# Performance work log

Hardware: AMD Instinct MI355X
Metric: run time of the kernel (lower is better)

Reference implementation:

```python
import jax, jax.numpy as jnp
import numpy as np

N, E, B = 10000, 160000, 256
IN, DESC = 57, 1217
# (in_dim, heads, out_per_head) for the 4 GATConv layers
CONV_DIMS = [(57, 5, 114), (570, 5, 171), (855, 5, 114), (570, 1, 570)]
FC_DIMS = [(1024 + DESC, 1024), (1024, 2048), (2048, 1024), (1024, 256), (256, 1)]


def setup_inputs() -> dict:
    key = jax.random.key(0)
    cnt = [0]
    def p(shape, scale=0.05):
        cnt[0] += 1
        return jax.random.normal(jax.random.fold_in(key, cnt[0]), shape, jnp.float32) * scale
    d = {}
    d["x"] = jax.random.normal(jax.random.fold_in(key, 100), (N, IN), jnp.float32)
    d["edge_index"] = jax.random.randint(jax.random.fold_in(key, 101), (2, E), 0, N)
    d["batch"] = jnp.sort(jax.random.randint(jax.random.fold_in(key, 102), (N,), 0, B))
    d["desc"] = jax.random.normal(jax.random.fold_in(key, 103), (B, DESC), jnp.float32)
    for i, (ci, H, C) in enumerate(CONV_DIMS, 1):
        d[f"W{i}"] = p((ci, H * C))
        d[f"as{i}"] = p((H, C))
        d[f"ad{i}"] = p((H, C))
        d[f"b{i}"] = jnp.zeros((H * C,), jnp.float32)
    d["Wg"] = p((570, 1024)); d["bg"] = jnp.zeros((1024,), jnp.float32)
    for i, (ci, co) in enumerate(FC_DIMS, 1):
        d[f"Wf{i}"] = p((ci, co))
        d[f"bf{i}"] = jnp.zeros((co,), jnp.float32)
    return d


def gat_conv(x, src, dst, W, a_src, a_dst, b):
    """PyG GATConv (eval mode: attention dropout off), self-loops already in src/dst."""
    n = x.shape[0]
    H, C = a_src.shape
    h = (x @ W).reshape(n, H, C)                      # [N,H,C]
    al_s = (h * a_src).sum(-1)                         # [N,H]
    al_d = (h * a_dst).sum(-1)                         # [N,H]
    e = jax.nn.leaky_relu(al_s[src] + al_d[dst], 0.2)  # [E,H]
    # segment softmax over destination node
    m = jax.ops.segment_max(e, dst, num_segments=n)
    e = jnp.exp(e - m[dst])
    s = jax.ops.segment_sum(e, dst, num_segments=n)
    alpha = e / (s[dst] + 1e-16)                       # [E,H]
    msg = h[src] * alpha[:, :, None]                   # [E,H,C]
    out = jax.ops.segment_sum(msg, dst, num_segments=n)
    return out.reshape(n, H * C) + b


def reference(x, edge_index, batch, desc,
              W1, as1, ad1, b1, W2, as2, ad2, b2,
              W3, as3, ad3, b3, W4, as4, ad4, b4,
              Wg, bg, Wf1, bf1, Wf2, bf2, Wf3, bf3, Wf4, bf4, Wf5, bf5):
    n = x.shape[0]
    loops = jnp.arange(n)
    src = jnp.concatenate([edge_index[0], loops])
    dst = jnp.concatenate([edge_index[1], loops])
    h = x
    for W, a_s, a_d, b in [(W1, as1, ad1, b1), (W2, as2, ad2, b2),
                           (W3, as3, ad3, b3), (W4, as4, ad4, b4)]:
        h = jax.nn.relu(gat_conv(h, src, dst, W, a_s, a_d, b))
    pooled = jax.ops.segment_sum(h, batch, num_segments=B)   # global_add_pool [B,570]
    g = pooled @ Wg + bg
    z = jnp.concatenate([g, desc], axis=1)                    # [B, 2241]
    z = jax.nn.relu(z @ Wf1 + bf1)
    z = jax.nn.relu(z @ Wf2 + bf2)
    z = jax.nn.relu(z @ Wf3 + bf3)
    z = jax.nn.relu(z @ Wf4 + bf4)
    return z @ Wf5 + bf5                                      # [B,1]
```

## Files before the change

### kernel.cpp

```cpp
#include <hip/hip_runtime.h>
#include <hip/hip_bf16.h>
#include <math.h>

#define NNODES 10000
#define NEDGES 160000
#define NB     256
#define ETOT   (NEDGES + NNODES)
#define INDIM  57
#define DESCD  1217

static inline size_t align256(size_t x) { return (x + 255) & ~size_t(255); }

typedef _Float16 half8_t __attribute__((ext_vector_type(8)));
typedef float f32x4 __attribute__((ext_vector_type(4)));

__device__ inline float wave_max(float v) {
#pragma unroll
  for (int o = 32; o > 0; o >>= 1) v = fmaxf(v, __shfl_xor(v, o));
  return v;
}
__device__ inline float wave_sum(float v) {
#pragma unroll
  for (int o = 32; o > 0; o >>= 1) v += __shfl_xor(v, o);
  return v;
}

__global__ void count_kernel(const int* __restrict__ ei, int* __restrict__ deg) {
  int e = blockIdx.x * blockDim.x + threadIdx.x;
  if (e < ETOT) {
    int dst = (e < NEDGES) ? ei[NEDGES + e] : (e - NEDGES);
    atomicAdd(&deg[dst], 1);
  }
}

__global__ __launch_bounds__(1024) void scan_kernel(const int* __restrict__ deg,
                                                    int* __restrict__ row_ptr,
                                                    int* __restrict__ cursor) {
  __shared__ int part[1024];
  const int CHUNK = (NNODES + 1023) / 1024;
  int t = threadIdx.x;
  int start = t * CHUNK;
  int sum = 0;
  for (int i = 0; i < CHUNK; ++i) {
    int idx = start + i;
    if (idx < NNODES) sum += deg[idx];
  }
  part[t] = sum;
  __syncthreads();
  for (int off = 1; off < 1024; off <<= 1) {
    int v = (t >= off) ? part[t - off] : 0;
    __syncthreads();
    part[t] += v;
    __syncthreads();
  }
  int run = (t > 0) ? part[t - 1] : 0;
  for (int i = 0; i < CHUNK; ++i) {
    int idx = start + i;
    if (idx < NNODES) {
      row_ptr[idx] = run;
      cursor[idx] = run;
      run += deg[idx];
    }
  }
  if (t == 1023) row_ptr[NNODES] = ETOT;
}

__global__ void scatter_kernel(const int* __restrict__ ei, int* __restrict__ cursor,
                               int* __restrict__ csr_src) {
  int e = blockIdx.x * blockDim.x + threadIdx.x;
  if (e < ETOT) {
    int src, dst;
    if (e < NEDGES) { src = ei[e]; dst = ei[NEDGES + e]; }
    else            { src = e - NEDGES; dst = src; }
    int idx = atomicAdd(&cursor[dst], 1);
    csr_src[idx] = src;
  }
}

__global__ void convert_x_kernel(const float* __restrict__ x, _Float16* __restrict__ x16) {
  int t = blockIdx.x * blockDim.x + threadIdx.x;
  if (t >= NNODES * 64) return;
  int n = t >> 6, k = t & 63;
  x16[t] = (_Float16)((k < INDIM) ? x[n * INDIM + k] : 0.f);
}

__global__ void convert_wt_kernel(const float* __restrict__ W, _Float16* __restrict__ Wt,
                                  int K, int N, int Kpad, int Npad) {
  int t = blockIdx.x * blockDim.x + threadIdx.x;
  if (t >= Npad * Kpad) return;
  int n = t / Kpad, k = t - n * Kpad;
  float v = (n < N && k < K) ? W[(size_t)k * N + n] : 0.f;
  Wt[t] = (_Float16)v;
}

__global__ void pooled16_kernel(const float* __restrict__ pooled, _Float16* __restrict__ p16) {
  int t = blockIdx.x * blockDim.x + threadIdx.x;
  if (t >= NB * 576) return;
  int b = t / 576, c = t - b * 576;
  p16[t] = (_Float16)((c < 570) ? pooled[b * 570 + c] : 0.f);
}

__global__ void desc_fill_kernel(const float* __restrict__ desc, _Float16* __restrict__ z16) {
  int t = blockIdx.x * blockDim.x + threadIdx.x;
  if (t >= NB * 1280) return;
  int b = t / 1280, i = t - b * 1280;
  z16[(size_t)b * 2304 + 1024 + i] = (_Float16)((i < DESCD) ? desc[b * DESCD + i] : 0.f);
}

__global__ __launch_bounds__(256) void mfma_gemm_kernel(
    const _Float16* __restrict__ A, const _Float16* __restrict__ Bt,
    _Float16* __restrict__ C, int M, int Kpad, int Nreal, int ldc) {
  __shared__ __align__(16) char smem[32768];
  char* AsB = smem;
  char* BsB = smem + 16384;
  int tid = threadIdx.x;
  int lane = tid & 63, wid = tid >> 6;
  int l15 = lane & 15, g = lane >> 4;
  int wr = wid >> 1, wc = wid & 1;
  int m0 = blockIdx.y * 128, n0 = blockIdx.x * 128;
  f32x4 acc[4][4];
#pragma unroll
  for (int i = 0; i < 4; ++i)
#pragma unroll
    for (int j = 0; j < 4; ++j) acc[i][j] = (f32x4){0.f, 0.f, 0.f, 0.f};

  int KT = Kpad >> 6;
  half8_t pa[4], pb[4];
#pragma unroll
  for (int i = 0; i < 4; ++i) {
    int r = i * 32 + (tid >> 3);
    int cs = (tid & 7) ^ (r & 7);
    int ga = min(m0 + r, M - 1);
    pa[i] = *(const half8_t*)(A + (size_t)ga * Kpad + cs * 8);
    pb[i] = *(const half8_t*)(Bt + (size_t)(n0 + r) * Kpad + cs * 8);
  }
  for (int kt = 0; kt < KT; ++kt) {
    __syncthreads();
#pragma unroll
    for (int i = 0; i < 4; ++i) {
      *(half8_t*)(AsB + i * 4096 + tid * 16) = pa[i];
      *(half8_t*)(BsB + i * 4096 + tid * 16) = pb[i];
    }
    __syncthreads();
    if (kt + 1 < KT) {
      int k0 = (kt + 1) << 6;
#pragma unroll
      for (int i = 0; i < 4; ++i) {
        int r = i * 32 + (tid >> 3);
        int cs = (tid & 7) ^ (r & 7);
        int ga = min(m0 + r, M - 1);
        pa[i] = *(const half8_t*)(A + (size_t)ga * Kpad + k0 + cs * 8);
        pb[i] = *(const half8_t*)(Bt + (size_t)(n0 + r) * Kpad + k0 + cs * 8);
      }
    }
#pragma unroll
    for (int kk = 0; kk < 2; ++kk) {
      half8_t af[4], bf[4];
#pragma unroll
      for (int f = 0; f < 4; ++f) {
        int ra = wr * 64 + f * 16 + l15;
        af[f] = *(const half8_t*)(AsB + ra * 128 + (((kk * 4 + g) ^ (ra & 7)) << 4));
        int cb = wc * 64 + f * 16 + l15;
        bf[f] = *(const half8_t*)(BsB + cb * 128 + (((kk * 4 + g) ^ (cb & 7)) << 4));
      }
#pragma unroll
      for (int fm = 0; fm < 4; ++fm)
#pragma unroll
        for (int fn = 0; fn < 4; ++fn)
          acc[fm][fn] = __builtin_amdgcn_mfma_f32_16x16x32_f16(af[fm], bf[fn], acc[fm][fn], 0, 0, 0);
    }
  }
#pragma unroll
  for (int fm = 0; fm < 4; ++fm) {
    int gmb = m0 + wr * 64 + fm * 16 + g * 4;
#pragma unroll
    for (int fn = 0; fn < 4; ++fn) {
      int gn = n0 + wc * 64 + fn * 16 + l15;
      if (gn >= Nreal) continue;
#pragma unroll
      for (int j = 0; j < 4; ++j) {
        int gm = gmb + j;
        if (gm < M) C[(size_t)gm * ldc + gn] = (_Float16)acc[fm][fn][j];
      }
    }
  }
}

__global__ __launch_bounds__(256) void mfma_splitk_kernel(
    const _Float16* __restrict__ A, const _Float16* __restrict__ Bt,
    float* __restrict__ P, int M, int Kpad, int N, int ktpc) {
  __shared__ __align__(16) char smem[32768];
  char* AsB = smem;
  char* BsB = smem + 16384;
  int tid = threadIdx.x;
  int lane = tid & 63, wid = tid >> 6;
  int l15 = lane & 15, g = lane >> 4;
  int wr = wid >> 1, wc = wid & 1;
  int m0 = blockIdx.y * 128, n0 = blockIdx.x * 128;
  int z = blockIdx.z;
  int KT = Kpad >> 6;
  int ktb = z * ktpc;
  int kte = min(KT, ktb + ktpc);
  f32x4 acc[4][4];
#pragma unroll
  for (int i = 0; i < 4; ++i)
#pragma unroll
    for (int j = 0; j < 4; ++j) acc[i][j] = (f32x4){0.f, 0.f, 0.f, 0.f};

  half8_t pa[4], pb[4];
  {
    int k0 = ktb << 6;
#pragma unroll
    for (int i = 0; i < 4; ++i) {
      int r = i * 32 + (tid >> 3);
      int cs = (tid & 7) ^ (r & 7);
      int ga = min(m0 + r, M - 1);
      pa[i] = *(const half8_t*)(A + (size_t)ga * Kpad + k0 + cs * 8);
      pb[i] = *(const half8_t*)(Bt + (size_t)(n0 + r) * Kpad + k0 + cs * 8);
    }
  }
  for (int kt = ktb; kt < kte; ++kt) {
    __syncthreads();
#pragma unroll
    for (int i = 0; i < 4; ++i) {
      *(half8_t*)(AsB + i * 4096 + tid * 16) = pa[i];
      *(half8_t*)(BsB + i * 4096 + tid * 16) = pb[i];
    }
    __syncthreads();
    if (kt + 1 < kte) {
      int k0 = (kt + 1) << 6;
#pragma unroll
      for (int i = 0; i < 4; ++i) {
        int r = i * 32 + (tid >> 3);
        int cs = (tid & 7) ^ (r & 7);
        int ga = min(m0 + r, M - 1);
        pa[i] = *(const half8_t*)(A + (size_t)ga * Kpad + k0 + cs * 8);
        pb[i] = *(const half8_t*)(Bt + (size_t)(n0 + r) * Kpad + k0 + cs * 8);
      }
    }
#pragma unroll
    for (int kk = 0; kk < 2; ++kk) {
      half8_t af[4], bf[4];
#pragma unroll
      for (int f = 0; f < 4; ++f) {
        int ra = wr * 64 + f * 16 + l15;
        af[f] = *(const half8_t*)(AsB + ra * 128 + (((kk * 4 + g) ^ (ra & 7)) << 4));
        int cb = wc * 64 + f * 16 + l15;
        bf[f] = *(const half8_t*)(BsB + cb * 128 + (((kk * 4 + g) ^ (cb & 7)) << 4));
      }
#pragma unroll
      for (int fm = 0; fm < 4; ++fm)
#pragma unroll
        for (int fn = 0; fn < 4; ++fn)
          acc[fm][fn] = __builtin_amdgcn_mfma_f32_16x16x32_f16(af[fm], bf[fn], acc[fm][fn], 0, 0, 0);
    }
  }
  size_t zb = (size_t)z * M;
#pragma unroll
  for (int fm = 0; fm < 4; ++fm) {
    int gmb = m0 + wr * 64 + fm * 16 + g * 4;
#pragma unroll
    for (int fn = 0; fn < 4; ++fn) {
      int gn = n0 + wc * 64 + fn * 16 + l15;
      if (gn >= N) continue;
#pragma unroll
      for (int j = 0; j < 4; ++j) {
        int gm = gmb + j;
        if (gm < M) P[(zb + gm) * N + gn] = acc[fm][fn][j];
      }
    }
  }
}

__global__ void reduce16_kernel(const float* __restrict__ P, const float* __restrict__ bias,
                                _Float16* __restrict__ O, int M, int N, int ldo,
                                int S, int relu) {
  int idx = blockIdx.x * blockDim.x + threadIdx.x;
  if (idx >= M * ldo) return;
  int row = idx / ldo, col = idx - row * ldo;
  if (col >= N) return;
  float s = bias[col];
  int MN = M * N;
  for (int z = 0; z < S; ++z) s += P[(size_t)z * MN + row * N + col];
  if (relu) s = fmaxf(s, 0.f);
  O[idx] = (_Float16)s;
}

__global__ __launch_bounds__(256) void fc5_kernel(const _Float16* __restrict__ A,
                                                  const float* __restrict__ w,
                                                  const float* __restrict__ b,
                                                  float* __restrict__ out) {
  int wid = threadIdx.x >> 6, lane = threadIdx.x & 63;
  int m = blockIdx.x * 4 + wid;
  if (m >= NB) return;
  float s = 0.f;
  for (int k = lane; k < 256; k += 64) s += (float)A[m * 256 + k] * w[k];
  s = wave_sum(s);
  if (lane == 0) out[m] = s + b[0];
}

__global__ __launch_bounds__(256) void al_kernel(const _Float16* __restrict__ hbuf,
                                                 const float* __restrict__ a_s,
                                                 const float* __restrict__ a_d,
                                                 float* __restrict__ als,
                                                 float* __restrict__ ald,
                                                 int H, int C, int ldh) {
  int wid = threadIdx.x >> 6, lane = threadIdx.x & 63;
  int g = blockIdx.x * 4 + wid;
  if (g >= NNODES * H) return;
  int n = g / H, h = g % H;
  const _Float16* hr = hbuf + (size_t)n * ldh + (size_t)h * C;
  float ss = 0.f, sd = 0.f;
  for (int c = lane; c < C; c += 64) {
    float v = (float)hr[c];
    ss += v * a_s[h * C + c];
    sd += v * a_d[h * C + c];
  }
  ss = wave_sum(ss);
  sd = wave_sum(sd);
  if (lane == 0) { als[g] = ss; ald[g] = sd; }
}

template <int H>
__global__ __launch_bounds__(256) void att_kernel_t(const float* __restrict__ als,
                                                    const float* __restrict__ ald,
                                                    const int* __restrict__ row_ptr,
                                                    const int* __restrict__ csr_src,
                                                    float* __restrict__ alpha) {
  int wid = threadIdx.x >> 6, lane = threadIdx.x & 63;
  int n = blockIdx.x * 4 + wid;
  if (n >= NNODES) return;
  int rp = row_ptr[n], deg = row_ptr[n + 1] - rp;
  float ad[H], m[H], e0[H], e1[H], ssum[H];
#pragma unroll
  for (int h = 0; h < H; ++h) { ad[h] = ald[n * H + h]; m[h] = -1e30f; ssum[h] = 0.f; }
  for (int j = lane, it = 0; j < deg; j += 64, ++it) {
    int s = csr_src[rp + j];
#pragma unroll
    for (int h = 0; h < H; ++h) {
      float e = als[s * H + h] + ad[h];
      e = (e >= 0.f) ? e : 0.2f * e;
      if (it == 0) e0[h] = e; else if (it == 1) e1[h] = e;
      m[h] = fmaxf(m[h], e);
    }
  }
#pragma unroll
  for (int h = 0; h < H; ++h) m[h] = wave_max(m[h]);
  for (int j = lane, it = 0; j < deg; j += 64, ++it) {
    int s = (it >= 2) ? csr_src[rp + j] : 0;
#pragma unroll
    for (int h = 0; h < H; ++h) {
      float e;
      if (it == 0) e = e0[h];
      else if (it == 1) e = e1[h];
      else { e = als[s * H + h] + ad[h]; e = (e >= 0.f) ? e : 0.2f * e; }
      ssum[h] += expf(e - m[h]);
    }
  }
#pragma unroll
  for (int h = 0; h < H; ++h) { ssum[h] = 1.f / (wave_sum(ssum[h]) + 1e-16f); }
  for (int j = lane, it = 0; j < deg; j += 64, ++it) {
    int s = (it >= 2) ? csr_src[rp + j] : 0;
#pragma unroll
    for (int h = 0; h < H; ++h) {
      float e;
      if (it == 0) e = e0[h];
      else if (it == 1) e = e1[h];
      else { e = als[s * H + h] + ad[h]; e = (e >= 0.f) ? e : 0.2f * e; }
      alpha[(size_t)(rp + j) * H + h] = expf(e - m[h]) * ssum[h];
    }
  }
}

__global__ __launch_bounds__(256) void agg_kernel(const _Float16* __restrict__ hbuf,
                                                  const float* __restrict__ alpha,
                                                  const int* __restrict__ row_ptr,
                                                  const int* __restrict__ csr_src,
                                                  const float* __restrict__ bias,
                                                  _Float16* __restrict__ h16o,
                                                  int H, int C, int ldh, int ldo,
                                                  int HC, int nchunks) {
  int wid = threadIdx.x >> 6, lane = threadIdx.x & 63;
  int gw = blockIdx.x * 4 + wid;
  int n = gw / nchunks, chunk = gw - n * nchunks;
  if (n >= NNODES) return;
  int k0 = chunk * 512 + lane * 8;
  if (k0 >= ldo) return;
  _Float16* op = h16o + (size_t)n * ldo + k0;
  if (k0 >= HC) { *(half8_t*)op = (half8_t){}; return; }
  int h0 = k0 / C;
  int h1 = min(k0 + 7, HC - 1) / C;
  int split = (h0 + 1) * C;
  int rp = row_ptr[n], deg = row_ptr[n + 1] - rp;
  float acc[8] = {};
#pragma unroll 2
  for (int j = 0; j < deg; ++j) {
    int e = rp + j;
    int s = csr_src[e];
    float a0 = alpha[(size_t)e * H + h0];
    float a1 = alpha[(size_t)e * H + h1];
    half8_t v = *(const half8_t*)(hbuf + (size_t)s * ldh + k0);
#pragma unroll
    for (int i = 0; i < 8; ++i)
      acc[i] += ((k0 + i < split) ? a0 : a1) * (float)v[i];
  }
  half8_t o;
#pragma unroll
  for (int i = 0; i < 8; ++i)
    o[i] = (_Float16)((k0 + i < HC) ? fmaxf(acc[i] + bias[k0 + i], 0.f) : 0.f);
  *(half8_t*)op = o;
}

__global__ __launch_bounds__(256) void pool_kernel(const _Float16* __restrict__ h4,
                                                   const int* __restrict__ batch,
                                                   float* __restrict__ pooled, int F, int ldh) {
  int wid = threadIdx.x >> 6, lane = threadIdx.x & 63;
  int n = blockIdx.x * 4 + wid;
  if (n >= NNODES) return;
  int b = batch[n];
  for (int k = lane; k < F; k += 64)
    atomicAdd(&pooled[(size_t)b * F + k], (float)h4[(size_t)n * ldh + k]);
}

extern "C" void kernel_launch(void* const* d_in, const int* in_sizes, int n_in,
                              void* d_out, int out_size, void* d_ws, size_t ws_size,
                              hipStream_t stream) {
  const float* x    = (const float*)d_in[0];
  const int*   ei   = (const int*)d_in[1];
  const int*   batch= (const int*)d_in[2];
  const float* desc = (const float*)d_in[3];
  const float* W1 = (const float*)d_in[4];  const float* as1 = (const float*)d_in[5];
  const float* ad1 = (const float*)d_in[6]; const float* b1 = (const float*)d_in[7];
  const float* W2 = (const float*)d_in[8];  const float* as2 = (const float*)d_in[9];
  const float* ad2 = (const float*)d_in[10];const float* b2 = (const float*)d_in[11];
  const float* W3 = (const float*)d_in[12]; const float* as3 = (const float*)d_in[13];
  const float* ad3 = (const float*)d_in[14];const float* b3 = (const float*)d_in[15];
  const float* W4 = (const float*)d_in[16]; const float* as4 = (const float*)d_in[17];
  const float* ad4 = (const float*)d_in[18];const float* b4 = (const float*)d_in[19];
  const float* Wg = (const float*)d_in[20]; const float* bg = (const float*)d_in[21];
  const float* Wf1 = (const float*)d_in[22];const float* bf1 = (const float*)d_in[23];
  const float* Wf2 = (const float*)d_in[24];const float* bf2 = (const float*)d_in[25];
  const float* Wf3 = (const float*)d_in[26];const float* bf3 = (const float*)d_in[27];
  const float* Wf4 = (const float*)d_in[28];const float* bf4 = (const float*)d_in[29];
  const float* Wf5 = (const float*)d_in[30];const float* bf5 = (const float*)d_in[31];
  float* out = (float*)d_out;

  char* p = (char*)d_ws;
  size_t off = 0;
  auto alloc = [&](size_t bytes) -> char* {
    char* r = p + off;
    off = align256(off + bytes);
    return r;
  };
  int*      deg     = (int*)alloc(sizeof(int) * NNODES);
  int*      row_ptr = (int*)alloc(sizeof(int) * (NNODES + 1));
  int*      cursor  = (int*)alloc(sizeof(int) * NNODES);
  int*      csr_src = (int*)alloc(sizeof(int) * ETOT);
  float*    als     = (float*)alloc(sizeof(float) * NNODES * 5);
  float*    ald     = (float*)alloc(sizeof(float) * NNODES * 5);
  float*    alpha   = (float*)alloc(sizeof(float) * (size_t)ETOT * 5);
  _Float16* x16     = (_Float16*)alloc(sizeof(_Float16) * (size_t)NNODES * 64);
  _Float16* hA16    = (_Float16*)alloc(sizeof(_Float16) * ((size_t)NNODES * 856 + 1024));
  _Float16* h16     = (_Float16*)alloc(sizeof(_Float16) * ((size_t)NNODES * 896 + 1024));
  _Float16* Wt      = (_Float16*)alloc(sizeof(_Float16) * 1024 * 2304);
  float*    pooled  = (float*)alloc(sizeof(float) * NB * 570);
  _Float16* p16     = (_Float16*)alloc(sizeof(_Float16) * NB * 576);
  _Float16* z16     = (_Float16*)alloc(sizeof(_Float16) * NB * 2304);
  _Float16* t16     = (_Float16*)alloc(sizeof(_Float16) * NB * 2048);
  _Float16* u16     = (_Float16*)alloc(sizeof(_Float16) * NB * 2048);
  _Float16* v16     = (_Float16*)alloc(sizeof(_Float16) * NB * 256);
  (void)ws_size;

  hipMemsetAsync(deg, 0, sizeof(int) * NNODES, stream);
  {
    dim3 g((ETOT + 255) / 256);
    count_kernel<<<g, 256, 0, stream>>>(ei, deg);
    scan_kernel<<<1, 1024, 0, stream>>>(deg, row_ptr, cursor);
    scatter_kernel<<<g, 256, 0, stream>>>(ei, cursor, csr_src);
  }
  convert_x_kernel<<<(NNODES * 64 + 255) / 256, 256, 0, stream>>>(x, x16);

  dim3 gnode((NNODES + 3) / 4);

  struct LayerDef { const float* W; const float* a_s; const float* a_d; const float* b;
                    int K; int H; int C; int Kpad; int Npad; int ldh; int ldo; };
  LayerDef L[4] = {
    { W1, as1, ad1, b1, INDIM, 5, 114,  64, 640, 572, 576 },
    { W2, as2, ad2, b2, 570,   5, 171, 576, 896, 856, 896 },
    { W3, as3, ad3, b3, 855,   5, 114, 896, 640, 572, 576 },
    { W4, as4, ad4, b4, 570,   1, 570, 576, 640, 572, 576 },
  };
  for (int l = 0; l < 4; ++l) {
    int HC = L[l].H * L[l].C;
    {
      int tot = L[l].Npad * L[l].Kpad;
      convert_wt_kernel<<<(tot + 255) / 256, 256, 0, stream>>>(L[l].W, Wt, L[l].K, HC,
                                                               L[l].Kpad, L[l].Npad);
    }
    {
      const _Float16* Ain = (l == 0) ? x16 : h16;
      dim3 g(L[l].Npad / 128, (NNODES + 127) / 128);
      mfma_gemm_kernel<<<g, 256, 0, stream>>>(Ain, Wt, hA16, NNODES, L[l].Kpad, HC, L[l].ldh);
    }
    {
      dim3 g((NNODES * L[l].H + 3) / 4);
      al_kernel<<<g, 256, 0, stream>>>(hA16, L[l].a_s, L[l].a_d, als, ald, L[l].H, L[l].C, L[l].ldh);
    }
    if (L[l].H == 5)
      att_kernel_t<5><<<gnode, 256, 0, stream>>>(als, ald, row_ptr, csr_src, alpha);
    else
      att_kernel_t<1><<<gnode, 256, 0, stream>>>(als, ald, row_ptr, csr_src, alpha);
    {
      int nchunks = (L[l].ldo + 511) / 512;
      dim3 g((NNODES * nchunks + 3) / 4);
      agg_kernel<<<g, 256, 0, stream>>>(hA16, alpha, row_ptr, csr_src, L[l].b, h16,
                                        L[l].H, L[l].C, L[l].ldh, L[l].ldo, HC, nchunks);
    }
  }

  hipMemsetAsync(pooled, 0, sizeof(float) * NB * 570, stream);
  pool_kernel<<<gnode, 256, 0, stream>>>(h16, batch, pooled, 570, 576);

  float* partials = (float*)hA16;
  auto head_gemm = [&](const _Float16* A, const float* W, const float* bias,
                       _Float16* O, int K, int Kpad, int N, int ldo, int relu,
                       int ktpc, int S) {
    int tot = N * Kpad;
    convert_wt_kernel<<<(tot + 255) / 256, 256, 0, stream>>>(W, Wt, K, N, Kpad, N);
    dim3 g(N / 128, NB / 128, S);
    mfma_splitk_kernel<<<g, 256, 0, stream>>>(A, Wt, partials, NB, Kpad, N, ktpc);
    int totO = NB * ldo;
    reduce16_kernel<<<(totO + 255) / 256, 256, 0, stream>>>(partials, bias, O, NB, N, ldo, S, relu);
  };

  pooled16_kernel<<<(NB * 576 + 255) / 256, 256, 0, stream>>>(pooled, p16);
  head_gemm(p16, Wg, bg, z16, 570, 576, 1024, 2304, 0, 3, 3);
  desc_fill_kernel<<<(NB * 1280 + 255) / 256, 256, 0, stream>>>(desc, z16);
  head_gemm(z16, Wf1, bf1, t16, 1024 + DESCD, 2304, 1024, 1024, 1, 3, 12);
  head_gemm(t16, Wf2, bf2, u16, 1024, 1024, 2048, 2048, 1, 2, 8);
  head_gemm(u16, Wf3, bf3, t16, 2048, 2048, 1024, 1024, 1, 2, 16);
  head_gemm(t16, Wf4, bf4, v16, 1024, 1024, 256, 256, 1, 1, 16);
  fc5_kernel<<<(NB + 3) / 4, 256, 0, stream>>>(v16, Wf5, bf5, out);
}
```

Before: 539.3 us.

## Fold attention projections into GEMM weights and batch weight conversion kernels

```diff
diff --git a/kernel.cpp b/kernel.cpp
--- a/kernel.cpp
+++ b/kernel.cpp
@@ -84,13 +84,53 @@
   x16[t] = (_Float16)((k < INDIM) ? x[n * INDIM + k] : 0.f);
 }
 
-__global__ void convert_wt_kernel(const float* __restrict__ W, _Float16* __restrict__ Wt,
-                                  int K, int N, int Kpad, int Npad) {
+struct LW { const float* W; const float* as; const float* ad; _Float16* dst;
+            int K, HC, Kpad, Npad, C, H, la; };
+
+__global__ void prep_layerw_kernel(LW d0, LW d1, LW d2, LW d3,
+                                   int c1, int c2, int c3, int c4) {
   int t = blockIdx.x * blockDim.x + threadIdx.x;
-  if (t >= Npad * Kpad) return;
-  int n = t / Kpad, k = t - n * Kpad;
-  float v = (n < N && k < K) ? W[(size_t)k * N + n] : 0.f;
-  Wt[t] = (_Float16)v;
+  LW d; int base;
+  if (t < c1)      { d = d0; base = 0; }
+  else if (t < c2) { d = d1; base = c1; }
+  else if (t < c3) { d = d2; base = c2; }
+  else if (t < c4) { d = d3; base = c3; }
+  else return;
+  int idx = t - base;
+  int k = idx / d.Npad, n = idx - k * d.Npad;
+  float v = 0.f;
+  if (k < d.K) {
+    if (n < d.HC) {
+      v = d.W[(size_t)k * d.HC + n];
+    } else if (n >= d.la && n < d.la + 2 * d.H) {
+      int h = n - d.la;
+      const float* a = d.as;
+      if (h >= d.H) { h -= d.H; a = d.ad; }
+      float s = 0.f;
+      for (int c = 0; c < d.C; ++c)
+        s += d.W[(size_t)k * d.HC + h * d.C + c] * a[h * d.C + c];
+      v = s;
+    }
+  }
+  d.dst[(size_t)n * d.Kpad + k] = (_Float16)v;
+}
+
+struct HW { const float* W; _Float16* dst; int K, N, Kpad; };
+
+__global__ void prep_headw_kernel(HW d0, HW d1, HW d2, HW d3, HW d4,
+                                  int c1, int c2, int c3, int c4, int c5) {
+  int t = blockIdx.x * blockDim.x + threadIdx.x;
+  HW d; int base;
+  if (t < c1)      { d = d0; base = 0; }
+  else if (t < c2) { d = d1; base = c1; }
+  else if (t < c3) { d = d2; base = c2; }
+  else if (t < c4) { d = d3; base = c3; }
+  else if (t < c5) { d = d4; base = c4; }
+  else return;
+  int idx = t - base;
+  int k = idx / d.N, n = idx - k * d.N;
+  float v = (k < d.K) ? d.W[(size_t)k * d.N + n] : 0.f;
+  d.dst[(size_t)n * d.Kpad + k] = (_Float16)v;
 }
 
 __global__ void pooled16_kernel(const float* __restrict__ pooled, _Float16* __restrict__ p16) {
@@ -299,46 +339,28 @@
   if (lane == 0) out[m] = s + b[0];
 }
 
-__global__ __launch_bounds__(256) void al_kernel(const _Float16* __restrict__ hbuf,
-                                                 const float* __restrict__ a_s,
-                                                 const float* __restrict__ a_d,
-                                                 float* __restrict__ als,
-                                                 float* __restrict__ ald,
-                                                 int H, int C, int ldh) {
-  int wid = threadIdx.x >> 6, lane = threadIdx.x & 63;
-  int g = blockIdx.x * 4 + wid;
-  if (g >= NNODES * H) return;
-  int n = g / H, h = g % H;
-  const _Float16* hr = hbuf + (size_t)n * ldh + (size_t)h * C;
-  float ss = 0.f, sd = 0.f;
-  for (int c = lane; c < C; c += 64) {
-    float v = (float)hr[c];
-    ss += v * a_s[h * C + c];
-    sd += v * a_d[h * C + c];
-  }
-  ss = wave_sum(ss);
-  sd = wave_sum(sd);
-  if (lane == 0) { als[g] = ss; ald[g] = sd; }
-}
-
 template <int H>
-__global__ __launch_bounds__(256) void att_kernel_t(const float* __restrict__ als,
-                                                    const float* __restrict__ ald,
+__global__ __launch_bounds__(256) void att_kernel_t(const _Float16* __restrict__ hbuf,
+                                                    int ldh, int la,
                                                     const int* __restrict__ row_ptr,
                                                     const int* __restrict__ csr_src,
-                                                    float* __restrict__ alpha) {
+                                                    float* __restrict__ alpha_t) {
   int wid = threadIdx.x >> 6, lane = threadIdx.x & 63;
   int n = blockIdx.x * 4 + wid;
   if (n >= NNODES) return;
   int rp = row_ptr[n], deg = row_ptr[n + 1] - rp;
   float ad[H], m[H], e0[H], e1[H], ssum[H];
 #pragma unroll
-  for (int h = 0; h < H; ++h) { ad[h] = ald[n * H + h]; m[h] = -1e30f; ssum[h] = 0.f; }
+  for (int h = 0; h < H; ++h) {
+    ad[h] = (float)hbuf[(size_t)n * ldh + la + H + h];
+    m[h] = -1e30f; ssum[h] = 0.f;
+  }
   for (int j = lane, it = 0; j < deg; j += 64, ++it) {
     int s = csr_src[rp + j];
+    half8_t v = *(const half8_t*)(hbuf + (size_t)s * ldh + la);
 #pragma unroll
     for (int h = 0; h < H; ++h) {
-      float e = als[s * H + h] + ad[h];
+      float e = (float)v[h] + ad[h];
       e = (e >= 0.f) ? e : 0.2f * e;
       if (it == 0) e0[h] = e; else if (it == 1) e1[h] = e;
       m[h] = fmaxf(m[h], e);
@@ -347,33 +369,35 @@
 #pragma unroll
   for (int h = 0; h < H; ++h) m[h] = wave_max(m[h]);
   for (int j = lane, it = 0; j < deg; j += 64, ++it) {
-    int s = (it >= 2) ? csr_src[rp + j] : 0;
+    half8_t v{};
+    if (it >= 2) v = *(const half8_t*)(hbuf + (size_t)csr_src[rp + j] * ldh + la);
 #pragma unroll
     for (int h = 0; h < H; ++h) {
       float e;
       if (it == 0) e = e0[h];
       else if (it == 1) e = e1[h];
-      else { e = als[s * H + h] + ad[h]; e = (e >= 0.f) ? e : 0.2f * e; }
+      else { e = (float)v[h] + ad[h]; e = (e >= 0.f) ? e : 0.2f * e; }
       ssum[h] += expf(e - m[h]);
     }
   }
 #pragma unroll
-  for (int h = 0; h < H; ++h) { ssum[h] = 1.f / (wave_sum(ssum[h]) + 1e-16f); }
+  for (int h = 0; h < H; ++h) ssum[h] = 1.f / (wave_sum(ssum[h]) + 1e-16f);
   for (int j = lane, it = 0; j < deg; j += 64, ++it) {
-    int s = (it >= 2) ? csr_src[rp + j] : 0;
+    half8_t v{};
+    if (it >= 2) v = *(const half8_t*)(hbuf + (size_t)csr_src[rp + j] * ldh + la);
 #pragma unroll
     for (int h = 0; h < H; ++h) {
       float e;
       if (it == 0) e = e0[h];
       else if (it == 1) e = e1[h];
-      else { e = als[s * H + h] + ad[h]; e = (e >= 0.f) ? e : 0.2f * e; }
-      alpha[(size_t)(rp + j) * H + h] = expf(e - m[h]) * ssum[h];
+      else { e = (float)v[h] + ad[h]; e = (e >= 0.f) ? e : 0.2f * e; }
+      alpha_t[(size_t)h * ETOT + rp + j] = expf(e - m[h]) * ssum[h];
     }
   }
 }
 
 __global__ __launch_bounds__(256) void agg_kernel(const _Float16* __restrict__ hbuf,
-                                                  const float* __restrict__ alpha,
+                                                  const float* __restrict__ alpha_t,
                                                   const int* __restrict__ row_ptr,
                                                   const int* __restrict__ csr_src,
                                                   const float* __restrict__ bias,
@@ -391,18 +415,43 @@
   int h0 = k0 / C;
   int h1 = min(k0 + 7, HC - 1) / C;
   int split = (h0 + 1) * C;
-  int rp = row_ptr[n], deg = row_ptr[n + 1] - rp;
+  const float* A0 = alpha_t + (size_t)h0 * ETOT;
+  const float* A1 = alpha_t + (size_t)h1 * ETOT;
+  int rp = row_ptr[n], re = row_ptr[n + 1];
   float acc[8] = {};
-#pragma unroll 2
-  for (int j = 0; j < deg; ++j) {
-    int e = rp + j;
-    int s = csr_src[e];
-    float a0 = alpha[(size_t)e * H + h0];
-    float a1 = alpha[(size_t)e * H + h1];
+  int j = rp;
+  for (; j < re && (j & 3); ++j) {
+    int s = csr_src[j];
+    float a0 = A0[j], a1 = A1[j];
     half8_t v = *(const half8_t*)(hbuf + (size_t)s * ldh + k0);
 #pragma unroll
-    for (int i = 0; i < 8; ++i)
-      acc[i] += ((k0 + i < split) ? a0 : a1) * (float)v[i];
+    for (int i = 0; i < 8; ++i) acc[i] += ((k0 + i < split) ? a0 : a1) * (float)v[i];
+  }
+  for (; j + 4 <= re; j += 4) {
+    int4 s4 = *(const int4*)(csr_src + j);
+    float4 a0v = *(const float4*)(A0 + j);
+    float4 a1v = *(const float4*)(A1 + j);
+    half8_t v0 = *(const half8_t*)(hbuf + (size_t)s4.x * ldh + k0);
+    half8_t v1 = *(const half8_t*)(hbuf + (size_t)s4.y * ldh + k0);
+    half8_t v2 = *(const half8_t*)(hbuf + (size_t)s4.z * ldh + k0);
+    half8_t v3 = *(const half8_t*)(hbuf + (size_t)s4.w * ldh + k0);
+#pragma unroll
+    for (int i = 0; i < 8; ++i) {
+      bool lo = (k0 + i < split);
+      float a = lo ? a0v.x : a1v.x;
+      float b = lo ? a0v.y : a1v.y;
+      float c = lo ? a0v.z : a1v.z;
+      float d = lo ? a0v.w : a1v.w;
+      acc[i] += a * (float)v0[i] + b * (float)v1[i];
+      acc[i] += c * (float)v2[i] + d * (float)v3[i];
+    }
+  }
+  for (; j < re; ++j) {
+    int s = csr_src[j];
+    float a0 = A0[j], a1 = A1[j];
+    half8_t v = *(const half8_t*)(hbuf + (size_t)s * ldh + k0);
+#pragma unroll
+    for (int i = 0; i < 8; ++i) acc[i] += ((k0 + i < split) ? a0 : a1) * (float)v[i];
   }
   half8_t o;
 #pragma unroll
@@ -456,13 +505,19 @@
   int*      row_ptr = (int*)alloc(sizeof(int) * (NNODES + 1));
   int*      cursor  = (int*)alloc(sizeof(int) * NNODES);
   int*      csr_src = (int*)alloc(sizeof(int) * ETOT);
-  float*    als     = (float*)alloc(sizeof(float) * NNODES * 5);
-  float*    ald     = (float*)alloc(sizeof(float) * NNODES * 5);
-  float*    alpha   = (float*)alloc(sizeof(float) * (size_t)ETOT * 5);
+  float*    alpha_t = (float*)alloc(sizeof(float) * (size_t)5 * ETOT);
   _Float16* x16     = (_Float16*)alloc(sizeof(_Float16) * (size_t)NNODES * 64);
-  _Float16* hA16    = (_Float16*)alloc(sizeof(_Float16) * ((size_t)NNODES * 856 + 1024));
+  _Float16* hA16    = (_Float16*)alloc(sizeof(_Float16) * ((size_t)NNODES * 872 + 1024));
   _Float16* h16     = (_Float16*)alloc(sizeof(_Float16) * ((size_t)NNODES * 896 + 1024));
-  _Float16* Wt      = (_Float16*)alloc(sizeof(_Float16) * 1024 * 2304);
+  _Float16* WtL1 = (_Float16*)alloc(sizeof(_Float16) * 640 * 64);
+  _Float16* WtL2 = (_Float16*)alloc(sizeof(_Float16) * 896 * 576);
+  _Float16* WtL3 = (_Float16*)alloc(sizeof(_Float16) * 640 * 896);
+  _Float16* WtL4 = (_Float16*)alloc(sizeof(_Float16) * 640 * 576);
+  _Float16* WtG  = (_Float16*)alloc(sizeof(_Float16) * 1024 * 576);
+  _Float16* WtF1 = (_Float16*)alloc(sizeof(_Float16) * 1024 * 2304);
+  _Float16* WtF2 = (_Float16*)alloc(sizeof(_Float16) * 2048 * 1024);
+  _Float16* WtF3 = (_Float16*)alloc(sizeof(_Float16) * 1024 * 2048);
+  _Float16* WtF4 = (_Float16*)alloc(sizeof(_Float16) * 256 * 1024);
   float*    pooled  = (float*)alloc(sizeof(float) * NB * 570);
   _Float16* p16     = (_Float16*)alloc(sizeof(_Float16) * NB * 576);
   _Float16* z16     = (_Float16*)alloc(sizeof(_Float16) * NB * 2304);
@@ -480,41 +535,55 @@
   }
   convert_x_kernel<<<(NNODES * 64 + 255) / 256, 256, 0, stream>>>(x, x16);
 
+  {
+    LW l1 = { W1, as1, ad1, WtL1, INDIM, 570,  64, 640, 114, 5, 576 };
+    LW l2 = { W2, as2, ad2, WtL2, 570,   855, 576, 896, 171, 5, 856 };
+    LW l3 = { W3, as3, ad3, WtL3, 855,   570, 896, 640, 114, 5, 576 };
+    LW l4 = { W4, as4, ad4, WtL4, 570,   570, 576, 640, 570, 1, 576 };
+    int c1 = 640 * 64, c2 = c1 + 896 * 576, c3 = c2 + 640 * 896, c4 = c3 + 640 * 576;
+    prep_layerw_kernel<<<(c4 + 255) / 256, 256, 0, stream>>>(l1, l2, l3, l4, c1, c2, c3, c4);
+  }
+  {
+    HW h0 = { Wg,  WtG,  570,          1024,  576 };
+    HW h1 = { Wf1, WtF1, 1024 + DESCD, 1024, 2304 };
+    HW h2 = { Wf2, WtF2, 1024,         2048, 1024 };
+    HW h3 = { Wf3, WtF3, 2048,         1024, 2048 };
+    HW h4 = { Wf4, WtF4, 1024,          256, 1024 };
+    int c1 = 1024 * 576, c2 = c1 + 1024 * 2304, c3 = c2 + 2048 * 1024,
+        c4 = c3 + 1024 * 2048, c5 = c4 + 256 * 1024;
+    prep_headw_kernel<<<(c5 + 255) / 256, 256, 0, stream>>>(h0, h1, h2, h3, h4,
+                                                            c1, c2, c3, c4, c5);
+  }
+
   dim3 gnode((NNODES + 3) / 4);
 
-  struct LayerDef { const float* W; const float* a_s; const float* a_d; const float* b;
-                    int K; int H; int C; int Kpad; int Npad; int ldh; int ldo; };
+  struct LayerDef { _Float16* Wt; const float* b;
+                    int H, C, HC, Kpad, Npad, ldh, la, ldo; };
   LayerDef L[4] = {
-    { W1, as1, ad1, b1, INDIM, 5, 114,  64, 640, 572, 576 },
-    { W2, as2, ad2, b2, 570,   5, 171, 576, 896, 856, 896 },
-    { W3, as3, ad3, b3, 855,   5, 114, 896, 640, 572, 576 },
-    { W4, as4, ad4, b4, 570,   1, 570, 576, 640, 572, 576 },
+    { WtL1, b1, 5, 114, 570,  64, 640, 592, 576, 576 },
+    { WtL2, b2, 5, 171, 855, 576, 896, 872, 856, 896 },
+    { WtL3, b3, 5, 114, 570, 896, 640, 592, 576, 576 },
+    { WtL4, b4, 1, 570, 570, 576, 640, 592, 576, 576 },
   };
   for (int l = 0; l < 4; ++l) {
-    int HC = L[l].H * L[l].C;
-    {
-      int tot = L[l].Npad * L[l].Kpad;
-      convert_wt_kernel<<<(tot + 255) / 256, 256, 0, stream>>>(L[l].W, Wt, L[l].K, HC,
-                                                               L[l].Kpad, L[l].Npad);
-    }
+    int Nreal = L[l].la + 2 * L[l].H;
     {
       const _Float16* Ain = (l == 0) ? x16 : h16;
       dim3 g(L[l].Npad / 128, (NNODES + 127) / 128);
-      mfma_gemm_kernel<<<g, 256, 0, stream>>>(Ain, Wt, hA16, NNODES, L[l].Kpad, HC, L[l].ldh);
-    }
-    {
-      dim3 g((NNODES * L[l].H + 3) / 4);
-      al_kernel<<<g, 256, 0, stream>>>(hA16, L[l].a_s, L[l].a_d, als, ald, L[l].H, L[l].C, L[l].ldh);
+      mfma_gemm_kernel<<<g, 256, 0, stream>>>(Ain, L[l].Wt, hA16, NNODES, L[l].Kpad,
+                                              Nreal, L[l].ldh);
     }
     if (L[l].H == 5)
-      att_kernel_t<5><<<gnode, 256, 0, stream>>>(als, ald, row_ptr, csr_src, alpha);
+      att_kernel_t<5><<<gnode, 256, 0, stream>>>(hA16, L[l].ldh, L[l].la,
+                                                 row_ptr, csr_src, alpha_t);
     else
-      att_kernel_t<1><<<gnode, 256, 0, stream>>>(als, ald, row_ptr, csr_src, alpha);
+      att_kernel_t<1><<<gnode, 256, 0, stream>>>(hA16, L[l].ldh, L[l].la,
+                                                 row_ptr, csr_src, alpha_t);
     {
       int nchunks = (L[l].ldo + 511) / 512;
       dim3 g((NNODES * nchunks + 3) / 4);
-      agg_kernel<<<g, 256, 0, stream>>>(hA16, alpha, row_ptr, csr_src, L[l].b, h16,
-                                        L[l].H, L[l].C, L[l].ldh, L[l].ldo, HC, nchunks);
+      agg_kernel<<<g, 256, 0, stream>>>(hA16, alpha_t, row_ptr, csr_src, L[l].b, h16,
+                                        L[l].H, L[l].C, L[l].ldh, L[l].ldo, L[l].HC, nchunks);
     }
   }
 
@@ -522,11 +591,9 @@
   pool_kernel<<<gnode, 256, 0, stream>>>(h16, batch, pooled, 570, 576);
 
   float* partials = (float*)hA16;
-  auto head_gemm = [&](const _Float16* A, const float* W, const float* bias,
-                       _Float16* O, int K, int Kpad, int N, int ldo, int relu,
+  auto head_gemm = [&](const _Float16* A, const _Float16* Wt, const float* bias,
+                       _Float16* O, int Kpad, int N, int ldo, int relu,
                        int ktpc, int S) {
-    int tot = N * Kpad;
-    convert_wt_kernel<<<(tot + 255) / 256, 256, 0, stream>>>(W, Wt, K, N, Kpad, N);
     dim3 g(N / 128, NB / 128, S);
     mfma_splitk_kernel<<<g, 256, 0, stream>>>(A, Wt, partials, NB, Kpad, N, ktpc);
     int totO = NB * ldo;
@@ -534,11 +601,11 @@
   };
 
   pooled16_kernel<<<(NB * 576 + 255) / 256, 256, 0, stream>>>(pooled, p16);
-  head_gemm(p16, Wg, bg, z16, 570, 576, 1024, 2304, 0, 3, 3);
+  head_gemm(p16, WtG, bg, z16, 576, 1024, 2304, 0, 3, 3);
   desc_fill_kernel<<<(NB * 1280 + 255) / 256, 256, 0, stream>>>(desc, z16);
-  head_gemm(z16, Wf1, bf1, t16, 1024 + DESCD, 2304, 1024, 1024, 1, 3, 12);
-  head_gemm(t16, Wf2, bf2, u16, 1024, 1024, 2048, 2048, 1, 2, 8);
-  head_gemm(u16, Wf3, bf3, t16, 2048, 2048, 1024, 1024, 1, 2, 16);
-  head_gemm(t16, Wf4, bf4, v16, 1024, 1024, 256, 256, 1, 1, 16);
+  head_gemm(z16, WtF1, bf1, t16, 2304, 1024, 1024, 1, 3, 12);
+  head_gemm(t16, WtF2, bf2, u16, 1024, 2048, 2048, 1, 2, 8);
+  head_gemm(u16, WtF3, bf3, t16, 2048, 1024, 1024, 1, 2, 16);
+  head_gemm(t16, WtF4, bf4, v16, 1024,  256,  256, 1, 1, 16);
   fc5_kernel<<<(NB + 3) / 4, 256, 0, stream>>>(v16, Wf5, bf5, out);
 }
```

After: 552.4 us. 2.4% more time.
